# Optimization experiments

Hardware: AMD Instinct MI355X
Metric: run time of the kernel (lower is better)

The kernel has to match this reference:

```python
import jax, jax.numpy as jnp
import numpy as np

N, E, B = 10000, 100000, 64
IN_DIM, EDGE_DIM = 16, 8
HID = [32, 64]
OUT_DIM = 128
BN_EPS = 1e-5


def setup_inputs() -> dict:
    key = jax.random.key(0)
    ks = iter(jax.random.split(key, 32))
    inp = {}
    inp["x"] = jax.random.normal(next(ks), (N, IN_DIM), dtype=jnp.float32)
    inp["edge_index"] = jax.random.randint(next(ks), (2, E), 0, N, dtype=jnp.int64)
    inp["edge_attr"] = jax.random.normal(next(ks), (E, EDGE_DIM), dtype=jnp.float32)
    inp["batch"] = jnp.sort(jax.random.randint(next(ks), (N,), 0, B, dtype=jnp.int64))
    inp["edge_batch"] = jax.random.randint(next(ks), (E,), 0, B, dtype=jnp.int64)
    pre = IN_DIM
    for i, hd in enumerate(HID):
        s = 1.0 / np.sqrt(EDGE_DIM)
        inp[f"w_nn{i}"] = jax.random.uniform(next(ks), (pre * hd, EDGE_DIM), jnp.float32, -s, s)
        inp[f"b_nn{i}"] = jax.random.uniform(next(ks), (pre * hd,), jnp.float32, -s, s)
        inp[f"root{i}"] = jax.random.normal(next(ks), (pre, hd), dtype=jnp.float32) / np.sqrt(pre)
        inp[f"bias{i}"] = jnp.zeros((hd,), dtype=jnp.float32)
        inp[f"gamma{i}"] = jnp.ones((hd,), dtype=jnp.float32)
        inp[f"beta{i}"] = jnp.zeros((hd,), dtype=jnp.float32)
        pre = hd
    s = 1.0 / np.sqrt(pre)
    inp["s_w"] = jax.random.uniform(next(ks), (OUT_DIM, pre), jnp.float32, -s, s)
    inp["s_b"] = jax.random.uniform(next(ks), (OUT_DIM,), jnp.float32, -s, s)
    inp["t_w"] = jax.random.uniform(next(ks), (OUT_DIM, pre), jnp.float32, -s, s)
    inp["t_b"] = jax.random.uniform(next(ks), (OUT_DIM,), jnp.float32, -s, s)
    return inp


def _nnconv(x, edge_index, edge_attr, w_nn, b_nn, root, bias, out_dim):
    src, dst = edge_index[0], edge_index[1]
    # per-edge weight matrices [E, in_dim, out_dim]
    W = (edge_attr @ w_nn.T + b_nn).reshape(edge_attr.shape[0], -1, out_dim)
    msg = jnp.einsum('ei,eio->eo', x[src], W)  # gather + per-edge matmul
    agg = jax.ops.segment_sum(msg, dst, num_segments=N)  # scatter-add
    return agg + x @ root + bias


def _bn(x, gamma, beta):
    mu = jnp.mean(x, axis=0)
    var = jnp.mean((x - mu) ** 2, axis=0)  # biased var (torch BN training)
    return gamma * (x - mu) * jax.lax.rsqrt(var + BN_EPS) + beta


def reference(x, edge_index, edge_attr, batch, edge_batch,
              w_nn0, b_nn0, root0, bias0, gamma0, beta0,
              w_nn1, b_nn1, root1, bias1, gamma1, beta1,
              s_w, s_b, t_w, t_b):
    x = jax.nn.relu(_bn(_nnconv(x, edge_index, edge_attr, w_nn0, b_nn0, root0, bias0, HID[0]), gamma0, beta0))
    x = jax.nn.relu(_bn(_nnconv(x, edge_index, edge_attr, w_nn1, b_nn1, root1, bias1, HID[1]), gamma1, beta1))
    s_x = jnp.clip(x @ s_w.T + s_b, -30.0, 30.0)
    t_x = x @ t_w.T + t_b
    f_x = jax.nn.sigmoid(-s_x) * jnp.tanh(t_x)  # 1/(1+exp(s)) == sigmoid(-s)
    return jax.ops.segment_sum(f_x, batch, num_segments=B)
```

## Files before the change

### kernel.cpp

```cpp
#include <hip/hip_runtime.h>
#include <math.h>

#define NN 10000
#define NE 100000
#define BN_EPS 1e-5f

__global__ __launch_bounds__(256) void k_prep(
    const float* __restrict__ w0, const float* __restrict__ b0,
    const float* __restrict__ root0,
    const float* __restrict__ w1, const float* __restrict__ b1,
    const float* __restrict__ root1,
    const float* __restrict__ s_w, const float* __restrict__ t_w,
    float* __restrict__ wT0, float* __restrict__ wT1, float* __restrict__ wstT,
    float* __restrict__ st0, float* __restrict__ st1, float* __restrict__ out)
{
  int gid = blockIdx.x * 256 + threadIdx.x;
  int gsz = gridDim.x * 256;
  for (int idx = gid; idx < 16 * 320; idx += gsz) {
    int i = idx / 320, c = idx - i * 320;
    float v;
    if (c < 256)      v = w0[(i * 32 + (c & 31)) * 8 + (c >> 5)];
    else if (c < 288) v = b0[i * 32 + (c - 256)];
    else              v = root0[i * 32 + (c - 288)];
    wT0[idx] = v;
  }
  for (int idx = gid; idx < 32 * 640; idx += gsz) {
    int i = idx / 640, c = idx - i * 640;
    float v;
    if (c < 512)      v = w1[(i * 64 + (c & 63)) * 8 + (c >> 6)];
    else if (c < 576) v = b1[i * 64 + (c - 512)];
    else              v = root1[i * 64 + (c - 576)];
    wT1[idx] = v;
  }
  for (int idx = gid; idx < 64 * 256; idx += gsz) {
    int i = idx >> 8, o = idx & 255;
    wstT[idx] = (o < 128) ? s_w[o * 64 + i] : t_w[(o - 128) * 64 + i];
  }
  for (int idx = gid; idx < 64 * 128; idx += gsz) out[idx] = 0.f;
  if (gid < 64)  st0[gid] = 0.f;
  if (gid < 128) st1[gid] = 0.f;
}

__global__ __launch_bounds__(320) void k_node0(
    const float* __restrict__ x, const float* __restrict__ wT0,
    const float* __restrict__ bias0,
    float* __restrict__ G0, float* __restrict__ h0)
{
  int c = threadIdx.x;
  float wc[16];
#pragma unroll
  for (int i = 0; i < 16; ++i) wc[i] = wT0[i * 320 + c];
  float bi = (c >= 288) ? bias0[c - 288] : 0.f;

  int n0 = blockIdx.x * 20;
  for (int n = n0; n < n0 + 20; n += 2) {
    const float4* xa = (const float4*)(x + n * 16);
    float a0 = 0.f, a1 = 0.f;
#pragma unroll
    for (int q = 0; q < 4; ++q) {
      float4 v0 = xa[q], v1 = xa[q + 4];
      a0 = fmaf(v0.x, wc[4 * q + 0], a0); a1 = fmaf(v1.x, wc[4 * q + 0], a1);
      a0 = fmaf(v0.y, wc[4 * q + 1], a0); a1 = fmaf(v1.y, wc[4 * q + 1], a1);
      a0 = fmaf(v0.z, wc[4 * q + 2], a0); a1 = fmaf(v1.z, wc[4 * q + 2], a1);
      a0 = fmaf(v0.w, wc[4 * q + 3], a0); a1 = fmaf(v1.w, wc[4 * q + 3], a1);
    }
    if (c < 288) {
      G0[n * 288 + c]       = a0;
      G0[(n + 1) * 288 + c] = a1;
    } else {
      h0[n * 32 + (c - 288)]       = a0 + bi;
      h0[(n + 1) * 32 + (c - 288)] = a1 + bi;
    }
  }
}

__global__ __launch_bounds__(256) void k_edge0(
    const int* __restrict__ ei, const float* __restrict__ ea,
    const float* __restrict__ G0, float* __restrict__ h0)
{
  int tid = threadIdx.x;
  int e = blockIdx.x * 8 + (tid >> 5);
  if (e >= NE) return;
  int o = tid & 31;
  int src = ei[e], dst = ei[NE + e];
  const float* gr = G0 + src * 288;
  const float* er = ea + e * 8;
  float m = gr[256 + o];
#pragma unroll
  for (int k = 0; k < 8; ++k) m = fmaf(er[k], gr[k * 32 + o], m);
  unsafeAtomicAdd(&h0[dst * 32 + o], m);
}

template <int C>
__global__ __launch_bounds__(256) void k_stats(
    const float* __restrict__ h, float* __restrict__ st)
{
  const int RPB = 256 / C;
  int tid = threadIdx.x;
  int col = tid % C, rg = tid / C;
  float s1 = 0.f, s2 = 0.f;
  int step = gridDim.x * RPB;
  for (int n = blockIdx.x * RPB + rg; n < NN; n += step) {
    float v = h[n * C + col];
    s1 += v; s2 += v * v;
  }
  __shared__ float l1[256], l2[256];
  l1[tid] = s1; l2[tid] = s2;
  __syncthreads();
  if (tid < C) {
    for (int r = 1; r < RPB; ++r) { s1 += l1[r * C + tid]; s2 += l2[r * C + tid]; }
    unsafeAtomicAdd(&st[tid], s1);
    unsafeAtomicAdd(&st[C + tid], s2);
  }
}

__global__ __launch_bounds__(256) void k_x1(
    float* __restrict__ h0, const float* __restrict__ st0,
    const float* __restrict__ g0, const float* __restrict__ be0)
{
  __shared__ float sc[32], sh[32];
  int tid = threadIdx.x;
  if (tid < 32) {
    float mu  = st0[tid] * (1.0f / NN);
    float var = st0[32 + tid] * (1.0f / NN) - mu * mu;
    float s   = g0[tid] * rsqrtf(var + BN_EPS);
    sc[tid] = s;
    sh[tid] = be0[tid] - mu * s;
  }
  __syncthreads();
  const int NV = NN * 8;
  for (int i = blockIdx.x * 256 + tid; i < NV; i += gridDim.x * 256) {
    float4 v = ((const float4*)h0)[i];
    int c0 = (i * 4) & 31;
    v.x = fmaxf(fmaf(v.x, sc[c0],     sh[c0]),     0.f);
    v.y = fmaxf(fmaf(v.y, sc[c0 + 1], sh[c0 + 1]), 0.f);
    v.z = fmaxf(fmaf(v.z, sc[c0 + 2], sh[c0 + 2]), 0.f);
    v.w = fmaxf(fmaf(v.w, sc[c0 + 3], sh[c0 + 3]), 0.f);
    ((float4*)h0)[i] = v;
  }
}

__global__ __launch_bounds__(320) void k_node1(
    const float* __restrict__ x1, const float* __restrict__ wT1,
    const float* __restrict__ bias1,
    float* __restrict__ G1, float* __restrict__ h1)
{
  int t = threadIdx.x;
  float wa[32], wb[32];
#pragma unroll
  for (int i = 0; i < 32; ++i) {
    float2 w2 = *(const float2*)(wT1 + i * 640 + 2 * t);
    wa[i] = w2.x; wb[i] = w2.y;
  }
  float bia = 0.f, bib = 0.f;
  if (t >= 288) { bia = bias1[2 * (t - 288)]; bib = bias1[2 * (t - 288) + 1]; }

  int n0 = blockIdx.x * 20;
  for (int n = n0; n < n0 + 20; n += 2) {
    const float4* xa = (const float4*)(x1 + n * 32);
    float a00 = 0.f, a01 = 0.f, a10 = 0.f, a11 = 0.f;
#pragma unroll
    for (int q = 0; q < 8; ++q) {
      float4 v0 = xa[q], v1 = xa[q + 8];
      a00 = fmaf(v0.x, wa[4 * q + 0], a00); a01 = fmaf(v0.x, wb[4 * q + 0], a01);
      a00 = fmaf(v0.y, wa[4 * q + 1], a00); a01 = fmaf(v0.y, wb[4 * q + 1], a01);
      a00 = fmaf(v0.z, wa[4 * q + 2], a00); a01 = fmaf(v0.z, wb[4 * q + 2], a01);
      a00 = fmaf(v0.w, wa[4 * q + 3], a00); a01 = fmaf(v0.w, wb[4 * q + 3], a01);
      a10 = fmaf(v1.x, wa[4 * q + 0], a10); a11 = fmaf(v1.x, wb[4 * q + 0], a11);
      a10 = fmaf(v1.y, wa[4 * q + 1], a10); a11 = fmaf(v1.y, wb[4 * q + 1], a11);
      a10 = fmaf(v1.z, wa[4 * q + 2], a10); a11 = fmaf(v1.z, wb[4 * q + 2], a11);
      a10 = fmaf(v1.w, wa[4 * q + 3], a10); a11 = fmaf(v1.w, wb[4 * q + 3], a11);
    }
    if (t < 288) {
      *(float2*)(G1 + n * 576 + 2 * t)       = make_float2(a00, a01);
      *(float2*)(G1 + (n + 1) * 576 + 2 * t) = make_float2(a10, a11);
    } else {
      int o = 2 * (t - 288);
      *(float2*)(h1 + n * 64 + o)       = make_float2(a00 + bia, a01 + bib);
      *(float2*)(h1 + (n + 1) * 64 + o) = make_float2(a10 + bia, a11 + bib);
    }
  }
}

__global__ __launch_bounds__(256) void k_edge1(
    const int* __restrict__ ei, const float* __restrict__ ea,
    const float* __restrict__ G1, float* __restrict__ h1)
{
  int tid = threadIdx.x;
  int e = blockIdx.x * 4 + (tid >> 6);
  if (e >= NE) return;
  int o = tid & 63;
  int src = ei[e], dst = ei[NE + e];
  const float* gr = G1 + src * 576;
  const float* er = ea + e * 8;
  float m = gr[512 + o];
#pragma unroll
  for (int k = 0; k < 8; ++k) m = fmaf(er[k], gr[k * 64 + o], m);
  unsafeAtomicAdd(&h1[dst * 64 + o], m);
}

__global__ __launch_bounds__(256) void k_x2(
    float* __restrict__ h1, const float* __restrict__ st1,
    const float* __restrict__ g1, const float* __restrict__ be1)
{
  __shared__ float sc[64], sh[64];
  int tid = threadIdx.x;
  if (tid < 64) {
    float mu  = st1[tid] * (1.0f / NN);
    float var = st1[64 + tid] * (1.0f / NN) - mu * mu;
    float s   = g1[tid] * rsqrtf(var + BN_EPS);
    sc[tid] = s;
    sh[tid] = be1[tid] - mu * s;
  }
  __syncthreads();
  const int NV = NN * 16;
  for (int i = blockIdx.x * 256 + tid; i < NV; i += gridDim.x * 256) {
    float4 v = ((const float4*)h1)[i];
    int c0 = (i * 4) & 63;
    v.x = fmaxf(fmaf(v.x, sc[c0],     sh[c0]),     0.f);
    v.y = fmaxf(fmaf(v.y, sc[c0 + 1], sh[c0 + 1]), 0.f);
    v.z = fmaxf(fmaf(v.z, sc[c0 + 2], sh[c0 + 2]), 0.f);
    v.w = fmaxf(fmaf(v.w, sc[c0 + 3], sh[c0 + 3]), 0.f);
    ((float4*)h1)[i] = v;
  }
}

__global__ __launch_bounds__(256) void k_head(
    const float* __restrict__ x2, const float* __restrict__ wstT,
    const float* __restrict__ s_b, const float* __restrict__ t_b,
    const int* __restrict__ batch, float* __restrict__ out)
{
  int tid = threadIdx.x;
  int c = tid & 127, g = tid >> 7;
  int n0 = blockIdx.x * 40 + g * 20;
  int n1 = n0 + 20;
  if (n0 >= NN) return;
  if (n1 > NN) n1 = NN;

  float wsr[64], wtr[64];
#pragma unroll
  for (int k = 0; k < 64; ++k) {
    wsr[k] = wstT[k * 256 + c];
    wtr[k] = wstT[k * 256 + 128 + c];
  }
  float sb = s_b[c], tb = t_b[c];

  int bcur = batch[n0];
  float facc = 0.f;
  for (int n = n0; n < n1; ++n) {
    const float4* xr = (const float4*)(x2 + (size_t)n * 64);
    float as = 0.f, at = 0.f;
#pragma unroll
    for (int q = 0; q < 16; ++q) {
      float4 xv = xr[q];
      as = fmaf(xv.x, wsr[4 * q + 0], as); at = fmaf(xv.x, wtr[4 * q + 0], at);
      as = fmaf(xv.y, wsr[4 * q + 1], as); at = fmaf(xv.y, wtr[4 * q + 1], at);
      as = fmaf(xv.z, wsr[4 * q + 2], as); at = fmaf(xv.z, wtr[4 * q + 2], at);
      as = fmaf(xv.w, wsr[4 * q + 3], as); at = fmaf(xv.w, wtr[4 * q + 3], at);
    }
    float sv = fminf(30.f, fmaxf(-30.f, as + sb));
    float tv = at + tb;
    float f  = tanhf(tv) / (1.f + expf(sv));
    int b = batch[n];
    if (b != bcur) {
      unsafeAtomicAdd(&out[bcur * 128 + c], facc);
      bcur = b; facc = 0.f;
    }
    facc += f;
  }
  unsafeAtomicAdd(&out[bcur * 128 + c], facc);
}

extern "C" void kernel_launch(void* const* d_in, const int* in_sizes, int n_in,
                              void* d_out, int out_size, void* d_ws, size_t ws_size,
                              hipStream_t stream)
{
  const float* x     = (const float*)d_in[0];
  const int*   ei    = (const int*)d_in[1];
  const float* ea    = (const float*)d_in[2];
  const int*   batch = (const int*)d_in[3];
  const float* w0    = (const float*)d_in[5];
  const float* b0    = (const float*)d_in[6];
  const float* root0 = (const float*)d_in[7];
  const float* bias0 = (const float*)d_in[8];
  const float* g0    = (const float*)d_in[9];
  const float* be0   = (const float*)d_in[10];
  const float* w1    = (const float*)d_in[11];
  const float* b1    = (const float*)d_in[12];
  const float* root1 = (const float*)d_in[13];
  const float* bias1 = (const float*)d_in[14];
  const float* g1    = (const float*)d_in[15];
  const float* be1   = (const float*)d_in[16];
  const float* s_w   = (const float*)d_in[17];
  const float* s_b   = (const float*)d_in[18];
  const float* t_w   = (const float*)d_in[19];
  const float* t_b   = (const float*)d_in[20];
  float* out = (float*)d_out;

  float* ws   = (float*)d_ws;
  float* G0   = ws;  ws += 2880000;
  float* G1   = ws;  ws += 5760000;
  float* h0   = ws;  ws += 320000;
  float* h1   = ws;  ws += 640000;
  float* st0  = ws;  ws += 64;
  float* st1  = ws;  ws += 128;
  float* wstT = ws;  ws += 16384;
  float* wT0  = ws;  ws += 5120;
  float* wT1  = ws;  ws += 20480;

  hipLaunchKernelGGL(k_prep, dim3(64), dim3(256), 0, stream,
                     w0, b0, root0, w1, b1, root1, s_w, t_w,
                     wT0, wT1, wstT, st0, st1, out);
  hipLaunchKernelGGL(k_node0, dim3(500), dim3(320), 0, stream,
                     x, wT0, bias0, G0, h0);
  hipLaunchKernelGGL(k_edge0, dim3((NE + 7) / 8), dim3(256), 0, stream, ei, ea, G0, h0);
  hipLaunchKernelGGL(k_stats<32>, dim3(64), dim3(256), 0, stream, h0, st0);
  hipLaunchKernelGGL(k_x1, dim3(160), dim3(256), 0, stream, h0, st0, g0, be0);
  hipLaunchKernelGGL(k_node1, dim3(500), dim3(320), 0, stream,
                     h0, wT1, bias1, G1, h1);
  hipLaunchKernelGGL(k_edge1, dim3((NE + 3) / 4), dim3(256), 0, stream, ei, ea, G1, h1);
  hipLaunchKernelGGL(k_stats<64>, dim3(128), dim3(256), 0, stream, h1, st1);
  hipLaunchKernelGGL(k_x2, dim3(320), dim3(256), 0, stream, h1, st1, g1, be1);
  hipLaunchKernelGGL(k_head, dim3(250), dim3(256), 0, stream,
                     h1, wstT, s_b, t_b, batch, out);
}
```

Measured before the change: 212.1 us.

## Replace atomic edge scatter with CSR-by-destination gather aggregation

Builds a destination-sorted edge list (histogram, single-block scan, atomic fill) each call, then aggregates messages per node with float2 loads and wave shuffles instead of per-edge float atomics into h0/h1. The goal is to remove contended atomic traffic and get coalesced per-node writes. It adds three extra kernel launches, including a serial one-block scan, and per-node load imbalance with only 10 edges per node on average. Edge order within a node becomes nondeterministic, as it was before.

```diff
diff --git a/kernel.cpp b/kernel.cpp
--- a/kernel.cpp
+++ b/kernel.cpp
@@ -4,6 +4,7 @@
 #define NN 10000
 #define NE 100000
 #define BN_EPS 1e-5f
+
 
 __global__ __launch_bounds__(256) void k_prep(
     const float* __restrict__ w0, const float* __restrict__ b0,
@@ -12,7 +13,8 @@
     const float* __restrict__ root1,
     const float* __restrict__ s_w, const float* __restrict__ t_w,
     float* __restrict__ wT0, float* __restrict__ wT1, float* __restrict__ wstT,
-    float* __restrict__ st0, float* __restrict__ st1, float* __restrict__ out)
+    float* __restrict__ st0, float* __restrict__ st1, float* __restrict__ out,
+    int* __restrict__ cnt)
 {
   int gid = blockIdx.x * 256 + threadIdx.x;
   int gsz = gridDim.x * 256;
@@ -37,8 +39,59 @@
     wstT[idx] = (o < 128) ? s_w[o * 64 + i] : t_w[(o - 128) * 64 + i];
   }
   for (int idx = gid; idx < 64 * 128; idx += gsz) out[idx] = 0.f;
+  for (int idx = gid; idx < NN; idx += gsz) cnt[idx] = 0;
   if (gid < 64)  st0[gid] = 0.f;
   if (gid < 128) st1[gid] = 0.f;
+}
+
+__global__ __launch_bounds__(256) void k_hist(
+    const int* __restrict__ ei, int* __restrict__ cnt)
+{
+  int gid = blockIdx.x * 256 + threadIdx.x;
+  for (int e = gid; e < NE; e += gridDim.x * 256)
+    atomicAdd(&cnt[ei[NE + e]], 1);
+}
+
+__global__ __launch_bounds__(1024) void k_scan(
+    const int* __restrict__ cnt, int* __restrict__ off, int* __restrict__ cursor)
+{
+  __shared__ int part[1024];
+  int t = threadIdx.x;
+  int base = t * 10;
+  int loc[10];
+  int s = 0;
+#pragma unroll
+  for (int i = 0; i < 10; ++i) {
+    int idx = base + i;
+    int v = (idx < NN) ? cnt[idx] : 0;
+    loc[i] = s; s += v;
+  }
+  part[t] = s;
+  __syncthreads();
+  for (int d = 1; d < 1024; d <<= 1) {
+    int v = (t >= d) ? part[t - d] : 0;
+    __syncthreads();
+    part[t] += v;
+    __syncthreads();
+  }
+  int excl = (t > 0) ? part[t - 1] : 0;
+#pragma unroll
+  for (int i = 0; i < 10; ++i) {
+    int idx = base + i;
+    if (idx < NN) { int o = excl + loc[i]; off[idx] = o; cursor[idx] = o; }
+  }
+  if (t == 1023) off[NN] = part[1023];
+}
+
+__global__ __launch_bounds__(256) void k_fill(
+    const int* __restrict__ ei, int* __restrict__ cursor, int* __restrict__ elist)
+{
+  int gid = blockIdx.x * 256 + threadIdx.x;
+  for (int e = gid; e < NE; e += gridDim.x * 256) {
+    int dst = ei[NE + e];
+    int pos = atomicAdd(&cursor[dst], 1);
+    elist[pos] = e;
+  }
 }
 
 __global__ __launch_bounds__(320) void k_node0(
@@ -74,21 +127,39 @@
   }
 }
 
-__global__ __launch_bounds__(256) void k_edge0(
+__global__ __launch_bounds__(256) void k_agg0(
     const int* __restrict__ ei, const float* __restrict__ ea,
+    const int* __restrict__ off, const int* __restrict__ elist,
     const float* __restrict__ G0, float* __restrict__ h0)
 {
   int tid = threadIdx.x;
-  int e = blockIdx.x * 8 + (tid >> 5);
-  if (e >= NE) return;
-  int o = tid & 31;
-  int src = ei[e], dst = ei[NE + e];
-  const float* gr = G0 + src * 288;
-  const float* er = ea + e * 8;
-  float m = gr[256 + o];
-#pragma unroll
-  for (int k = 0; k < 8; ++k) m = fmaf(er[k], gr[k * 32 + o], m);
-  unsafeAtomicAdd(&h0[dst * 32 + o], m);
+  int node = blockIdx.x * 4 + (tid >> 6);
+  int q = (tid >> 4) & 3;
+  int o = (tid & 15) * 2;
+  int j0 = off[node], j1 = off[node + 1];
+  float a0 = 0.f, a1 = 0.f;
+  for (int j = j0 + q; j < j1; j += 4) {
+    int e = elist[j];
+    int src = ei[e];
+    const float* gr = G0 + src * 288;
+    const float* er = ea + e * 8;
+    float m0 = gr[256 + o], m1 = gr[257 + o];
+#pragma unroll
+    for (int k = 0; k < 8; ++k) {
+      float2 g = *(const float2*)(gr + k * 32 + o);
+      float ek = er[k];
+      m0 = fmaf(ek, g.x, m0);
+      m1 = fmaf(ek, g.y, m1);
+    }
+    a0 += m0; a1 += m1;
+  }
+  a0 += __shfl_xor(a0, 16); a1 += __shfl_xor(a1, 16);
+  a0 += __shfl_xor(a0, 32); a1 += __shfl_xor(a1, 32);
+  if (q == 0) {
+    float2* p = (float2*)(h0 + node * 32 + o);
+    float2 v = *p;
+    *p = make_float2(v.x + a0, v.y + a1);
+  }
 }
 
 template <int C>
@@ -182,21 +253,38 @@
   }
 }
 
-__global__ __launch_bounds__(256) void k_edge1(
+__global__ __launch_bounds__(256) void k_agg1(
     const int* __restrict__ ei, const float* __restrict__ ea,
+    const int* __restrict__ off, const int* __restrict__ elist,
     const float* __restrict__ G1, float* __restrict__ h1)
 {
   int tid = threadIdx.x;
-  int e = blockIdx.x * 4 + (tid >> 6);
-  if (e >= NE) return;
-  int o = tid & 63;
-  int src = ei[e], dst = ei[NE + e];
-  const float* gr = G1 + src * 576;
-  const float* er = ea + e * 8;
-  float m = gr[512 + o];
-#pragma unroll
-  for (int k = 0; k < 8; ++k) m = fmaf(er[k], gr[k * 64 + o], m);
-  unsafeAtomicAdd(&h1[dst * 64 + o], m);
+  int node = blockIdx.x * 4 + (tid >> 6);
+  int half = (tid >> 5) & 1;
+  int o = (tid & 31) * 2;
+  int j0 = off[node], j1 = off[node + 1];
+  float a0 = 0.f, a1 = 0.f;
+  for (int j = j0 + half; j < j1; j += 2) {
+    int e = elist[j];
+    int src = ei[e];
+    const float* gr = G1 + src * 576;
+    const float* er = ea + e * 8;
+    float m0 = gr[512 + o], m1 = gr[513 + o];
+#pragma unroll
+    for (int k = 0; k < 8; ++k) {
+      float2 g = *(const float2*)(gr + k * 64 + o);
+      float ek = er[k];
+      m0 = fmaf(ek, g.x, m0);
+      m1 = fmaf(ek, g.y, m1);
+    }
+    a0 += m0; a1 += m1;
+  }
+  a0 += __shfl_xor(a0, 32); a1 += __shfl_xor(a1, 32);
+  if (half == 0) {
+    float2* p = (float2*)(h1 + node * 64 + o);
+    float2 v = *p;
+    *p = make_float2(v.x + a0, v.y + a1);
+  }
 }
 
 __global__ __launch_bounds__(256) void k_x2(
@@ -307,18 +395,27 @@
   float* wstT = ws;  ws += 16384;
   float* wT0  = ws;  ws += 5120;
   float* wT1  = ws;  ws += 20480;
+  int* cnt    = (int*)ws;
+  int* off    = cnt + NN;
+  int* cursor = off + NN + 1;
+  int* elist  = cursor + NN;
 
   hipLaunchKernelGGL(k_prep, dim3(64), dim3(256), 0, stream,
                      w0, b0, root0, w1, b1, root1, s_w, t_w,
-                     wT0, wT1, wstT, st0, st1, out);
+                     wT0, wT1, wstT, st0, st1, out, cnt);
+  hipLaunchKernelGGL(k_hist, dim3(256), dim3(256), 0, stream, ei, cnt);
+  hipLaunchKernelGGL(k_scan, dim3(1), dim3(1024), 0, stream, cnt, off, cursor);
+  hipLaunchKernelGGL(k_fill, dim3(256), dim3(256), 0, stream, ei, cursor, elist);
   hipLaunchKernelGGL(k_node0, dim3(500), dim3(320), 0, stream,
                      x, wT0, bias0, G0, h0);
-  hipLaunchKernelGGL(k_edge0, dim3((NE + 7) / 8), dim3(256), 0, stream, ei, ea, G0, h0);
+  hipLaunchKernelGGL(k_agg0, dim3(2500), dim3(256), 0, stream,
+                     ei, ea, off, elist, G0, h0);
   hipLaunchKernelGGL(k_stats<32>, dim3(64), dim3(256), 0, stream, h0, st0);
   hipLaunchKernelGGL(k_x1, dim3(160), dim3(256), 0, stream, h0, st0, g0, be0);
   hipLaunchKernelGGL(k_node1, dim3(500), dim3(320), 0, stream,
                      h0, wT1, bias1, G1, h1);
-  hipLaunchKernelGGL(k_edge1, dim3((NE + 3) / 4), dim3(256), 0, stream, ei, ea, G1, h1);
+  hipLaunchKernelGGL(k_agg1, dim3(2500), dim3(256), 0, stream,
+                     ei, ea, off, elist, G1, h1);
   hipLaunchKernelGGL(k_stats<64>, dim3(128), dim3(256), 0, stream, h1, st1);
   hipLaunchKernelGGL(k_x2, dim3(320), dim3(256), 0, stream, h1, st1, g1, be1);
   hipLaunchKernelGGL(k_head, dim3(250), dim3(256), 0, stream,
```

New measurement: 244.3 us. 15.2% more time.

## Fuse BN+ReLU into consumer kernels and drop weight-prep kernel

Applied to the files above, without the earlier changes.

Removes the k_prep kernel by having k_node0, k_node1 and k_head read the raw weights directly with strided gathers, and moves the zeroing of out and the stats buffers into k_node0. The standalone BN-apply kernels k_x1 and k_x2 are removed. BN scale/shift plus ReLU are now applied on the fly as k_node1 and k_head load node features. This cuts three launches and two read-modify-write passes over the hidden activations. In exchange the weight loads are uncoalesced, and the BN math is recomputed for every consumer read.

```diff
diff --git a/kernel.cpp b/kernel.cpp
--- a/kernel.cpp
+++ b/kernel.cpp
@@ -5,52 +5,34 @@
 #define NE 100000
 #define BN_EPS 1e-5f
 
-__global__ __launch_bounds__(256) void k_prep(
+
+__global__ __launch_bounds__(320) void k_node0(
+    const float* __restrict__ x,
     const float* __restrict__ w0, const float* __restrict__ b0,
-    const float* __restrict__ root0,
-    const float* __restrict__ w1, const float* __restrict__ b1,
-    const float* __restrict__ root1,
-    const float* __restrict__ s_w, const float* __restrict__ t_w,
-    float* __restrict__ wT0, float* __restrict__ wT1, float* __restrict__ wstT,
-    float* __restrict__ st0, float* __restrict__ st1, float* __restrict__ out)
-{
-  int gid = blockIdx.x * 256 + threadIdx.x;
-  int gsz = gridDim.x * 256;
-  for (int idx = gid; idx < 16 * 320; idx += gsz) {
-    int i = idx / 320, c = idx - i * 320;
-    float v;
-    if (c < 256)      v = w0[(i * 32 + (c & 31)) * 8 + (c >> 5)];
-    else if (c < 288) v = b0[i * 32 + (c - 256)];
-    else              v = root0[i * 32 + (c - 288)];
-    wT0[idx] = v;
-  }
-  for (int idx = gid; idx < 32 * 640; idx += gsz) {
-    int i = idx / 640, c = idx - i * 640;
-    float v;
-    if (c < 512)      v = w1[(i * 64 + (c & 63)) * 8 + (c >> 6)];
-    else if (c < 576) v = b1[i * 64 + (c - 512)];
-    else              v = root1[i * 64 + (c - 576)];
-    wT1[idx] = v;
-  }
-  for (int idx = gid; idx < 64 * 256; idx += gsz) {
-    int i = idx >> 8, o = idx & 255;
-    wstT[idx] = (o < 128) ? s_w[o * 64 + i] : t_w[(o - 128) * 64 + i];
-  }
-  for (int idx = gid; idx < 64 * 128; idx += gsz) out[idx] = 0.f;
+    const float* __restrict__ root0, const float* __restrict__ bias0,
+    float* __restrict__ G0, float* __restrict__ h0,
+    float* __restrict__ out, float* __restrict__ st0, float* __restrict__ st1)
+{
+  int tid = threadIdx.x;
+  int gid = blockIdx.x * 320 + tid;
+  for (int i = gid; i < 64 * 128; i += 500 * 320) out[i] = 0.f;
   if (gid < 64)  st0[gid] = 0.f;
   if (gid < 128) st1[gid] = 0.f;
-}
-
-__global__ __launch_bounds__(320) void k_node0(
-    const float* __restrict__ x, const float* __restrict__ wT0,
-    const float* __restrict__ bias0,
-    float* __restrict__ G0, float* __restrict__ h0)
-{
-  int c = threadIdx.x;
+
+  int c = tid;
   float wc[16];
-#pragma unroll
-  for (int i = 0; i < 16; ++i) wc[i] = wT0[i * 320 + c];
-  float bi = (c >= 288) ? bias0[c - 288] : 0.f;
+  float bi = 0.f;
+  if (c < 256) {
+#pragma unroll
+    for (int i = 0; i < 16; ++i) wc[i] = w0[(i * 32 + (c & 31)) * 8 + (c >> 5)];
+  } else if (c < 288) {
+#pragma unroll
+    for (int i = 0; i < 16; ++i) wc[i] = b0[i * 32 + (c - 256)];
+  } else {
+#pragma unroll
+    for (int i = 0; i < 16; ++i) wc[i] = root0[i * 32 + (c - 288)];
+    bi = bias0[c - 288];
+  }
 
   int n0 = blockIdx.x * 20;
   for (int n = n0; n < n0 + 20; n += 2) {
@@ -114,68 +96,83 @@
   }
 }
 
-__global__ __launch_bounds__(256) void k_x1(
-    float* __restrict__ h0, const float* __restrict__ st0,
-    const float* __restrict__ g0, const float* __restrict__ be0)
+__global__ __launch_bounds__(320) void k_node1(
+    const float* __restrict__ h0raw,
+    const float* __restrict__ st0, const float* __restrict__ g0,
+    const float* __restrict__ be0,
+    const float* __restrict__ w1, const float* __restrict__ b1,
+    const float* __restrict__ root1, const float* __restrict__ bias1,
+    float* __restrict__ G1, float* __restrict__ h1)
 {
   __shared__ float sc[32], sh[32];
-  int tid = threadIdx.x;
-  if (tid < 32) {
-    float mu  = st0[tid] * (1.0f / NN);
-    float var = st0[32 + tid] * (1.0f / NN) - mu * mu;
-    float s   = g0[tid] * rsqrtf(var + BN_EPS);
-    sc[tid] = s;
-    sh[tid] = be0[tid] - mu * s;
+  int t = threadIdx.x;
+  if (t < 32) {
+    float mu  = st0[t] * (1.0f / NN);
+    float var = st0[32 + t] * (1.0f / NN) - mu * mu;
+    float s   = g0[t] * rsqrtf(var + BN_EPS);
+    sc[t] = s;
+    sh[t] = be0[t] - mu * s;
   }
   __syncthreads();
-  const int NV = NN * 8;
-  for (int i = blockIdx.x * 256 + tid; i < NV; i += gridDim.x * 256) {
-    float4 v = ((const float4*)h0)[i];
-    int c0 = (i * 4) & 31;
-    v.x = fmaxf(fmaf(v.x, sc[c0],     sh[c0]),     0.f);
-    v.y = fmaxf(fmaf(v.y, sc[c0 + 1], sh[c0 + 1]), 0.f);
-    v.z = fmaxf(fmaf(v.z, sc[c0 + 2], sh[c0 + 2]), 0.f);
-    v.w = fmaxf(fmaf(v.w, sc[c0 + 3], sh[c0 + 3]), 0.f);
-    ((float4*)h0)[i] = v;
-  }
-}
-
-__global__ __launch_bounds__(320) void k_node1(
-    const float* __restrict__ x1, const float* __restrict__ wT1,
-    const float* __restrict__ bias1,
-    float* __restrict__ G1, float* __restrict__ h1)
-{
-  int t = threadIdx.x;
+
   float wa[32], wb[32];
-#pragma unroll
-  for (int i = 0; i < 32; ++i) {
-    float2 w2 = *(const float2*)(wT1 + i * 640 + 2 * t);
-    wa[i] = w2.x; wb[i] = w2.y;
-  }
   float bia = 0.f, bib = 0.f;
-  if (t >= 288) { bia = bias1[2 * (t - 288)]; bib = bias1[2 * (t - 288) + 1]; }
+  {
+    int cA = 2 * t;
+    if (cA < 512) {
+#pragma unroll
+      for (int i = 0; i < 32; ++i) {
+        int r = i * 64 + (cA & 63);
+        wa[i] = w1[r * 8 + (cA >> 6)];
+        wb[i] = w1[(r + 1) * 8 + (cA >> 6)];
+      }
+    } else if (cA < 576) {
+#pragma unroll
+      for (int i = 0; i < 32; ++i) {
+        wa[i] = b1[i * 64 + (cA - 512)];
+        wb[i] = b1[i * 64 + (cA - 511)];
+      }
+    } else {
+#pragma unroll
+      for (int i = 0; i < 32; ++i) {
+        wa[i] = root1[i * 64 + (cA - 576)];
+        wb[i] = root1[i * 64 + (cA - 575)];
+      }
+      bia = bias1[cA - 576];
+      bib = bias1[cA - 575];
+    }
+  }
 
   int n0 = blockIdx.x * 20;
   for (int n = n0; n < n0 + 20; n += 2) {
-    const float4* xa = (const float4*)(x1 + n * 32);
+    const float4* xa = (const float4*)(h0raw + n * 32);
     float a00 = 0.f, a01 = 0.f, a10 = 0.f, a11 = 0.f;
 #pragma unroll
     for (int q = 0; q < 8; ++q) {
       float4 v0 = xa[q], v1 = xa[q + 8];
-      a00 = fmaf(v0.x, wa[4 * q + 0], a00); a01 = fmaf(v0.x, wb[4 * q + 0], a01);
-      a00 = fmaf(v0.y, wa[4 * q + 1], a00); a01 = fmaf(v0.y, wb[4 * q + 1], a01);
-      a00 = fmaf(v0.z, wa[4 * q + 2], a00); a01 = fmaf(v0.z, wb[4 * q + 2], a01);
-      a00 = fmaf(v0.w, wa[4 * q + 3], a00); a01 = fmaf(v0.w, wb[4 * q + 3], a01);
-      a10 = fmaf(v1.x, wa[4 * q + 0], a10); a11 = fmaf(v1.x, wb[4 * q + 0], a11);
-      a10 = fmaf(v1.y, wa[4 * q + 1], a10); a11 = fmaf(v1.y, wb[4 * q + 1], a11);
-      a10 = fmaf(v1.z, wa[4 * q + 2], a10); a11 = fmaf(v1.z, wb[4 * q + 2], a11);
-      a10 = fmaf(v1.w, wa[4 * q + 3], a10); a11 = fmaf(v1.w, wb[4 * q + 3], a11);
+      int c0 = 4 * q;
+      v0.x = fmaxf(fmaf(v0.x, sc[c0],     sh[c0]),     0.f);
+      v0.y = fmaxf(fmaf(v0.y, sc[c0 + 1], sh[c0 + 1]), 0.f);
+      v0.z = fmaxf(fmaf(v0.z, sc[c0 + 2], sh[c0 + 2]), 0.f);
+      v0.w = fmaxf(fmaf(v0.w, sc[c0 + 3], sh[c0 + 3]), 0.f);
+      v1.x = fmaxf(fmaf(v1.x, sc[c0],     sh[c0]),     0.f);
+      v1.y = fmaxf(fmaf(v1.y, sc[c0 + 1], sh[c0 + 1]), 0.f);
+      v1.z = fmaxf(fmaf(v1.z, sc[c0 + 2], sh[c0 + 2]), 0.f);
+      v1.w = fmaxf(fmaf(v1.w, sc[c0 + 3], sh[c0 + 3]), 0.f);
+      a00 = fmaf(v0.x, wa[4*q+0], a00); a01 = fmaf(v0.x, wb[4*q+0], a01);
+      a00 = fmaf(v0.y, wa[4*q+1], a00); a01 = fmaf(v0.y, wb[4*q+1], a01);
+      a00 = fmaf(v0.z, wa[4*q+2], a00); a01 = fmaf(v0.z, wb[4*q+2], a01);
+      a00 = fmaf(v0.w, wa[4*q+3], a00); a01 = fmaf(v0.w, wb[4*q+3], a01);
+      a10 = fmaf(v1.x, wa[4*q+0], a10); a11 = fmaf(v1.x, wb[4*q+0], a11);
+      a10 = fmaf(v1.y, wa[4*q+1], a10); a11 = fmaf(v1.y, wb[4*q+1], a11);
+      a10 = fmaf(v1.z, wa[4*q+2], a10); a11 = fmaf(v1.z, wb[4*q+2], a11);
+      a10 = fmaf(v1.w, wa[4*q+3], a10); a11 = fmaf(v1.w, wb[4*q+3], a11);
     }
     if (t < 288) {
       *(float2*)(G1 + n * 576 + 2 * t)       = make_float2(a00, a01);
       *(float2*)(G1 + (n + 1) * 576 + 2 * t) = make_float2(a10, a11);
     } else {
-      int o = 2 * (t - 288);
+      int o = 2 * t - 576;
       *(float2*)(h1 + n * 64 + o)       = make_float2(a00 + bia, a01 + bib);
       *(float2*)(h1 + (n + 1) * 64 + o) = make_float2(a10 + bia, a11 + bib);
     }
@@ -199,9 +196,13 @@
   unsafeAtomicAdd(&h1[dst * 64 + o], m);
 }
 
-__global__ __launch_bounds__(256) void k_x2(
-    float* __restrict__ h1, const float* __restrict__ st1,
-    const float* __restrict__ g1, const float* __restrict__ be1)
+__global__ __launch_bounds__(256) void k_head(
+    const float* __restrict__ h1raw,
+    const float* __restrict__ st1, const float* __restrict__ g1,
+    const float* __restrict__ be1,
+    const float* __restrict__ s_w, const float* __restrict__ s_b,
+    const float* __restrict__ t_w, const float* __restrict__ t_b,
+    const int* __restrict__ batch, float* __restrict__ out)
 {
   __shared__ float sc[64], sh[64];
   int tid = threadIdx.x;
@@ -213,24 +214,7 @@
     sh[tid] = be1[tid] - mu * s;
   }
   __syncthreads();
-  const int NV = NN * 16;
-  for (int i = blockIdx.x * 256 + tid; i < NV; i += gridDim.x * 256) {
-    float4 v = ((const float4*)h1)[i];
-    int c0 = (i * 4) & 63;
-    v.x = fmaxf(fmaf(v.x, sc[c0],     sh[c0]),     0.f);
-    v.y = fmaxf(fmaf(v.y, sc[c0 + 1], sh[c0 + 1]), 0.f);
-    v.z = fmaxf(fmaf(v.z, sc[c0 + 2], sh[c0 + 2]), 0.f);
-    v.w = fmaxf(fmaf(v.w, sc[c0 + 3], sh[c0 + 3]), 0.f);
-    ((float4*)h1)[i] = v;
-  }
-}
-
-__global__ __launch_bounds__(256) void k_head(
-    const float* __restrict__ x2, const float* __restrict__ wstT,
-    const float* __restrict__ s_b, const float* __restrict__ t_b,
-    const int* __restrict__ batch, float* __restrict__ out)
-{
-  int tid = threadIdx.x;
+
   int c = tid & 127, g = tid >> 7;
   int n0 = blockIdx.x * 40 + g * 20;
   int n1 = n0 + 20;
@@ -238,21 +222,29 @@
   if (n1 > NN) n1 = NN;
 
   float wsr[64], wtr[64];
-#pragma unroll
-  for (int k = 0; k < 64; ++k) {
-    wsr[k] = wstT[k * 256 + c];
-    wtr[k] = wstT[k * 256 + 128 + c];
+  const float4* swp = (const float4*)(s_w + c * 64);
+  const float4* twp = (const float4*)(t_w + c * 64);
+#pragma unroll
+  for (int q = 0; q < 16; ++q) {
+    float4 a = swp[q], b = twp[q];
+    wsr[4*q+0] = a.x; wsr[4*q+1] = a.y; wsr[4*q+2] = a.z; wsr[4*q+3] = a.w;
+    wtr[4*q+0] = b.x; wtr[4*q+1] = b.y; wtr[4*q+2] = b.z; wtr[4*q+3] = b.w;
   }
   float sb = s_b[c], tb = t_b[c];
 
   int bcur = batch[n0];
   float facc = 0.f;
   for (int n = n0; n < n1; ++n) {
-    const float4* xr = (const float4*)(x2 + (size_t)n * 64);
+    const float4* xr = (const float4*)(h1raw + (size_t)n * 64);
     float as = 0.f, at = 0.f;
 #pragma unroll
     for (int q = 0; q < 16; ++q) {
       float4 xv = xr[q];
+      int c0 = 4 * q;
+      xv.x = fmaxf(fmaf(xv.x, sc[c0],     sh[c0]),     0.f);
+      xv.y = fmaxf(fmaf(xv.y, sc[c0 + 1], sh[c0 + 1]), 0.f);
+      xv.z = fmaxf(fmaf(xv.z, sc[c0 + 2], sh[c0 + 2]), 0.f);
+      xv.w = fmaxf(fmaf(xv.w, sc[c0 + 3], sh[c0 + 3]), 0.f);
       as = fmaf(xv.x, wsr[4 * q + 0], as); at = fmaf(xv.x, wtr[4 * q + 0], at);
       as = fmaf(xv.y, wsr[4 * q + 1], as); at = fmaf(xv.y, wtr[4 * q + 1], at);
       as = fmaf(xv.z, wsr[4 * q + 2], as); at = fmaf(xv.z, wtr[4 * q + 2], at);
@@ -304,23 +296,17 @@
   float* h1   = ws;  ws += 640000;
   float* st0  = ws;  ws += 64;
   float* st1  = ws;  ws += 128;
-  float* wstT = ws;  ws += 16384;
-  float* wT0  = ws;  ws += 5120;
-  float* wT1  = ws;  ws += 20480;
-
-  hipLaunchKernelGGL(k_prep, dim3(64), dim3(256), 0, stream,
-                     w0, b0, root0, w1, b1, root1, s_w, t_w,
-                     wT0, wT1, wstT, st0, st1, out);
+
   hipLaunchKernelGGL(k_node0, dim3(500), dim3(320), 0, stream,
-                     x, wT0, bias0, G0, h0);
-  hipLaunchKernelGGL(k_edge0, dim3((NE + 7) / 8), dim3(256), 0, stream, ei, ea, G0, h0);
+                     x, w0, b0, root0, bias0, G0, h0, out, st0, st1);
+  hipLaunchKernelGGL(k_edge0, dim3((NE + 7) / 8), dim3(256), 0, stream,
+                     ei, ea, G0, h0);
   hipLaunchKernelGGL(k_stats<32>, dim3(64), dim3(256), 0, stream, h0, st0);
-  hipLaunchKernelGGL(k_x1, dim3(160), dim3(256), 0, stream, h0, st0, g0, be0);
   hipLaunchKernelGGL(k_node1, dim3(500), dim3(320), 0, stream,
-                     h0, wT1, bias1, G1, h1);
-  hipLaunchKernelGGL(k_edge1, dim3((NE + 3) / 4), dim3(256), 0, stream, ei, ea, G1, h1);
+                     h0, st0, g0, be0, w1, b1, root1, bias1, G1, h1);
+  hipLaunchKernelGGL(k_edge1, dim3((NE + 3) / 4), dim3(256), 0, stream,
+                     ei, ea, G1, h1);
   hipLaunchKernelGGL(k_stats<64>, dim3(128), dim3(256), 0, stream, h1, st1);
-  hipLaunchKernelGGL(k_x2, dim3(320), dim3(256), 0, stream, h1, st1, g1, be1);
   hipLaunchKernelGGL(k_head, dim3(250), dim3(256), 0, stream,
-                     h1, wstT, s_b, t_b, batch, out);
-}
+                     h1, st1, g1, be1, s_w, s_b, t_w, t_b, batch, out);
+}
```

Result: slower. 243.0 us (+14.6%).
